# Optimization experiments

Hardware: AMD Instinct MI355X
Metric: run time of the kernel (lower is better)

The kernel has to match this reference:

```python
import jax, jax.numpy as jnp
import numpy as np

H = 64  # hidden_dim

def _gru_cell(x, h, Wih, Whh, bih, bhh):
    # PyTorch GRUCell math: gates ordered (r, z, n)
    gi = x @ Wih.T + bih            # [B, 3H]
    gh = h @ Whh.T + bhh            # [B, 3H]
    i_r, i_z, i_n = jnp.split(gi, 3, axis=-1)
    h_r, h_z, h_n = jnp.split(gh, 3, axis=-1)
    r = jax.nn.sigmoid(i_r + h_r)
    z = jax.nn.sigmoid(i_z + h_z)
    n = jnp.tanh(i_n + r * h_n)
    return (1.0 - z) * n + z * h

def setup_inputs() -> dict:
    key = jax.random.key(0)
    ks = jax.random.split(key, 13)
    B, T, D = 128, 512, 512
    x = jax.random.normal(ks[0], (B, T, D), dtype=jnp.float32)
    s = 1.0 / np.sqrt(H)
    def u(k, shape):
        return jax.random.uniform(k, shape, dtype=jnp.float32, minval=-s, maxval=s)
    return {
        "x": x,
        "W0ih": u(ks[1], (3 * H, D)), "W0hh": u(ks[2], (3 * H, H)),
        "b0ih": u(ks[3], (3 * H,)),   "b0hh": u(ks[4], (3 * H,)),
        "W1ih": u(ks[5], (3 * H, H)), "W1hh": u(ks[6], (3 * H, H)),
        "b1ih": u(ks[7], (3 * H,)),   "b1hh": u(ks[8], (3 * H,)),
        "W2ih": u(ks[9], (3 * H, H)), "W2hh": u(ks[10], (3 * H, H)),
        "b2ih": u(ks[11], (3 * H,)),  "b2hh": u(ks[12], (3 * H,)),
    }

def reference(x, W0ih, W0hh, b0ih, b0hh, W1ih, W1hh, b1ih, b1hh,
              W2ih, W2hh, b2ih, b2hh):
    # bContext=True path: per timestep, if the input slice has any nonzero,
    # run the 3 stacked GRU cells and emit h2; else keep states and emit zeros.
    B = x.shape[0]
    h_init = (jnp.zeros((B, H), x.dtype),) * 3

    def step(carry, xt):  # xt: [B, D]
        h0, h1, h2 = carry
        active = jnp.any(xt != 0)
        n0 = _gru_cell(xt, h0, W0ih, W0hh, b0ih, b0hh)
        n1 = _gru_cell(n0, h1, W1ih, W1hh, b1ih, b1hh)
        n2 = _gru_cell(n1, h2, W2ih, W2hh, b2ih, b2hh)
        h0 = jnp.where(active, n0, h0)
        h1 = jnp.where(active, n1, h1)
        h2 = jnp.where(active, n2, h2)
        out = jnp.where(active, h2, jnp.zeros_like(h2))
        return (h0, h1, h2), out

    xs = jnp.swapaxes(x, 0, 1)          # [T, B, D]
    _, outs = jax.lax.scan(step, h_init, xs)  # [T, B, H]
    return jnp.swapaxes(outs, 0, 1)     # [B, T, H]
```

## Files before the change

kernel.cpp:

```cpp
#include <hip/hip_runtime.h>

#define B_ 128
#define T_ 512
#define D_ 512
#define H_ 64
#define N3 192

#if __has_builtin(__builtin_amdgcn_rcpf)
#define RCP(x) __builtin_amdgcn_rcpf(x)
#else
#define RCP(x) (1.0f / (x))
#endif

typedef _Float16 h2v __attribute__((ext_vector_type(2)));
typedef _Float16 f16x8 __attribute__((ext_vector_type(8)));
typedef float f32x4 __attribute__((ext_vector_type(4)));

__device__ __forceinline__ float sigm_f(float x) {
  return RCP(1.0f + __expf(-x));
}
__device__ __forceinline__ float tanh_f(float x) {
  float e = __expf(-2.0f * fabsf(x));
  float t = (1.0f - e) * RCP(1.0f + e);
  return copysignf(t, x);
}

template <int CTRL>
__device__ __forceinline__ float dpp_add(float v) {
  int t = __builtin_amdgcn_update_dpp(0, __float_as_int(v), CTRL, 0xF, 0xF, true);
  return v + __int_as_float(t);
}
__device__ __forceinline__ float red2(float v) { return dpp_add<0xB1>(v); }
__device__ __forceinline__ float red4(float v) {
  v = dpp_add<0xB1>(v);
  v = dpp_add<0x4E>(v);
  return v;
}

__device__ __forceinline__ void dot4acc(int4 w, int4 h, float& s0, float& s1) {
  s0 = __builtin_amdgcn_fdot2(__builtin_bit_cast(h2v, w.x),
                              __builtin_bit_cast(h2v, h.x), s0, false);
  s1 = __builtin_amdgcn_fdot2(__builtin_bit_cast(h2v, w.y),
                              __builtin_bit_cast(h2v, h.y), s1, false);
  s0 = __builtin_amdgcn_fdot2(__builtin_bit_cast(h2v, w.z),
                              __builtin_bit_cast(h2v, h.z), s0, false);
  s1 = __builtin_amdgcn_fdot2(__builtin_bit_cast(h2v, w.w),
                              __builtin_bit_cast(h2v, h.w), s1, false);
}
__device__ __forceinline__ void dot8reg(const int* w, int4 a, int4 b,
                                        float& s0, float& s1) {
  s0 = __builtin_amdgcn_fdot2(__builtin_bit_cast(h2v, w[0]),
                              __builtin_bit_cast(h2v, a.x), s0, false);
  s1 = __builtin_amdgcn_fdot2(__builtin_bit_cast(h2v, w[1]),
                              __builtin_bit_cast(h2v, a.y), s1, false);
  s0 = __builtin_amdgcn_fdot2(__builtin_bit_cast(h2v, w[2]),
                              __builtin_bit_cast(h2v, a.z), s0, false);
  s1 = __builtin_amdgcn_fdot2(__builtin_bit_cast(h2v, w[3]),
                              __builtin_bit_cast(h2v, a.w), s1, false);
  s0 = __builtin_amdgcn_fdot2(__builtin_bit_cast(h2v, w[4]),
                              __builtin_bit_cast(h2v, b.x), s0, false);
  s1 = __builtin_amdgcn_fdot2(__builtin_bit_cast(h2v, w[5]),
                              __builtin_bit_cast(h2v, b.y), s1, false);
  s0 = __builtin_amdgcn_fdot2(__builtin_bit_cast(h2v, w[6]),
                              __builtin_bit_cast(h2v, b.z), s0, false);
  s1 = __builtin_amdgcn_fdot2(__builtin_bit_cast(h2v, w[7]),
                              __builtin_bit_cast(h2v, b.w), s1, false);
}

#define KEEP(x) asm volatile("" : "+v"(x))

__global__ __launch_bounds__(256) void gemm_kernel(
    const float* __restrict__ x,
    const float* __restrict__ w0ih,
    const float* __restrict__ b0ih,
    float* __restrict__ gi0,
    int* __restrict__ act,
    int t0, int Tc) {
  __shared__ _Float16 Xs[64][72];
  __shared__ _Float16 Ws[64][72];
  __shared__ unsigned char sflag[64];

  const int tid = threadIdx.x;
  const int bid = blockIdx.x;
  const int nt = bid % 3;
  const int mt = bid / 3;
  const int tpc = Tc >> 6;
  const int b  = mt / tpc;
  const int tt = mt % tpc;
  const int c0 = nt * 64;

  const int lane = tid & 63;
  const int wid  = tid >> 6;
  const int wm = (wid >> 1) * 32;
  const int wn = (wid & 1) * 32;
  const int l15 = lane & 15;
  const int l4  = lane >> 4;

  const float* xbase = x + ((size_t)b * T_ + t0 + tt * 64) * D_;
  const float* wbase = w0ih + (size_t)c0 * D_;

  const int srow = tid >> 2;
  const int scg  = (tid & 3) << 4;
  const float* xrow = xbase + (size_t)srow * D_;
  const float* wrow = wbase + (size_t)srow * D_;

  f32x4 acc[2][2];
#pragma unroll
  for (int mi = 0; mi < 2; ++mi)
#pragma unroll
    for (int ni = 0; ni < 2; ++ni) {
      acc[mi][ni].x = 0.f; acc[mi][ni].y = 0.f;
      acc[mi][ni].z = 0.f; acc[mi][ni].w = 0.f;
    }

  bool f = false;

  for (int kt = 0; kt < D_ / 64; ++kt) {
    const int k0 = kt * 64 + scg;
    float4 xa = *(const float4*)&xrow[k0];
    float4 xb = *(const float4*)&xrow[k0 + 4];
    float4 xc = *(const float4*)&xrow[k0 + 8];
    float4 xd = *(const float4*)&xrow[k0 + 12];
    float4 wa = *(const float4*)&wrow[k0];
    float4 wb = *(const float4*)&wrow[k0 + 4];
    float4 wc = *(const float4*)&wrow[k0 + 8];
    float4 wd = *(const float4*)&wrow[k0 + 12];
    f |= (xa.x != 0.f) | (xa.y != 0.f) | (xa.z != 0.f) | (xa.w != 0.f) |
         (xb.x != 0.f) | (xb.y != 0.f) | (xb.z != 0.f) | (xb.w != 0.f) |
         (xc.x != 0.f) | (xc.y != 0.f) | (xc.z != 0.f) | (xc.w != 0.f) |
         (xd.x != 0.f) | (xd.y != 0.f) | (xd.z != 0.f) | (xd.w != 0.f);
    __syncthreads();
    {
      f16x8 p0 = {(_Float16)xa.x, (_Float16)xa.y, (_Float16)xa.z, (_Float16)xa.w,
                  (_Float16)xb.x, (_Float16)xb.y, (_Float16)xb.z, (_Float16)xb.w};
      f16x8 p1 = {(_Float16)xc.x, (_Float16)xc.y, (_Float16)xc.z, (_Float16)xc.w,
                  (_Float16)xd.x, (_Float16)xd.y, (_Float16)xd.z, (_Float16)xd.w};
      *(f16x8*)&Xs[srow][scg] = p0;
      *(f16x8*)&Xs[srow][scg + 8] = p1;
      f16x8 q0 = {(_Float16)wa.x, (_Float16)wa.y, (_Float16)wa.z, (_Float16)wa.w,
                  (_Float16)wb.x, (_Float16)wb.y, (_Float16)wb.z, (_Float16)wb.w};
      f16x8 q1 = {(_Float16)wc.x, (_Float16)wc.y, (_Float16)wc.z, (_Float16)wc.w,
                  (_Float16)wd.x, (_Float16)wd.y, (_Float16)wd.z, (_Float16)wd.w};
      *(f16x8*)&Ws[srow][scg] = q0;
      *(f16x8*)&Ws[srow][scg + 8] = q1;
    }
    __syncthreads();
#pragma unroll
    for (int ks = 0; ks < 2; ++ks) {
      const int kb = ks * 32 + l4 * 8;
      f16x8 a0 = *(const f16x8*)&Xs[wm + l15][kb];
      f16x8 a1 = *(const f16x8*)&Xs[wm + 16 + l15][kb];
      f16x8 b0 = *(const f16x8*)&Ws[wn + l15][kb];
      f16x8 b1 = *(const f16x8*)&Ws[wn + 16 + l15][kb];
      acc[0][0] = __builtin_amdgcn_mfma_f32_16x16x32_f16(a0, b0, acc[0][0], 0, 0, 0);
      acc[0][1] = __builtin_amdgcn_mfma_f32_16x16x32_f16(a0, b1, acc[0][1], 0, 0, 0);
      acc[1][0] = __builtin_amdgcn_mfma_f32_16x16x32_f16(a1, b0, acc[1][0], 0, 0, 0);
      acc[1][1] = __builtin_amdgcn_mfma_f32_16x16x32_f16(a1, b1, acc[1][1], 0, 0, 0);
    }
  }

  const float bias0 = b0ih[c0 + wn + l15];
  const float bias1 = b0ih[c0 + wn + 16 + l15];
  const size_t rowbase = (size_t)b * Tc + tt * 64;
#pragma unroll
  for (int mi = 0; mi < 2; ++mi)
#pragma unroll
    for (int r = 0; r < 4; ++r) {
      const int m = wm + mi * 16 + l4 * 4 + r;
      float* orow = &gi0[(rowbase + m) * N3 + c0 + wn];
      orow[l15]      = acc[mi][0][r] + bias0;
      orow[16 + l15] = acc[mi][1][r] + bias1;
    }

  if (tid < 64) sflag[tid] = 0;
  __syncthreads();
  if (f) sflag[srow] = 1;
  __syncthreads();
  if (tid < 64 && sflag[tid]) act[t0 + tt * 64 + tid] = 1;
}

__global__ __launch_bounds__(640) void scan_kernel(
    const float* __restrict__ gi0,
    const float* __restrict__ w0hh, const float* __restrict__ w1ih,
    const float* __restrict__ w1hh, const float* __restrict__ w2ih,
    const float* __restrict__ w2hh,
    const float* __restrict__ b0hh, const float* __restrict__ b1ih,
    const float* __restrict__ b1hh, const float* __restrict__ b2ih,
    const float* __restrict__ b2hh,
    const int* __restrict__ act,
    float* __restrict__ hstate,
    float* __restrict__ out,
    int t0, int Tc) {
  const int b   = blockIdx.x;
  const int tid = threadIdx.x;

  __shared__ __align__(16) int4 s_w[3][192][8];
  __shared__ __align__(16) _Float16 s_h[3][2][H_];
  __shared__ int s_act[T_];

  {
    const float* wsrc[3] = {w0hh, w1hh, w2hh};
    for (int i = tid; i < 3 * 192 * 8; i += 640) {
      int m = i / 1536;
      int rem = i - m * 1536;
      int row = rem >> 3;
      int c = rem & 7;
      const float* sp = wsrc[m] + (size_t)row * H_ + 8 * c;
      float4 lo = *(const float4*)sp;
      float4 hi = *(const float4*)(sp + 4);
      h2v p0 = {(_Float16)lo.x, (_Float16)lo.y};
      h2v p1 = {(_Float16)lo.z, (_Float16)lo.w};
      h2v p2 = {(_Float16)hi.x, (_Float16)hi.y};
      h2v p3 = {(_Float16)hi.z, (_Float16)hi.w};
      int4 pk;
      pk.x = __builtin_bit_cast(int, p0);
      pk.y = __builtin_bit_cast(int, p1);
      pk.z = __builtin_bit_cast(int, p2);
      pk.w = __builtin_bit_cast(int, p3);
      s_w[m][row][c ^ (row & 7)] = pk;
    }
  }
  for (int i = tid; i < Tc; i += 640) s_act[i] = act[t0 + i];

  const int grp = (tid < 128) ? 0 : (tid < 384) ? 1 : 2;
  const int lt  = tid - ((grp == 0) ? 0 : (grp == 1) ? 128 : 384);
  const int jj  = (grp == 0) ? (lt >> 1) : (lt >> 2);
  const int gg  = (grp == 0) ? (lt & 1) : (lt & 3);
  const int swz = jj & 7;

  if (tid < H_) {
    float v0 = (t0 == 0) ? 0.f : hstate[0 * B_ * H_ + b * H_ + tid];
    float v1 = (t0 == 0) ? 0.f : hstate[1 * B_ * H_ + b * H_ + tid];
    float v2 = (t0 == 0) ? 0.f : hstate[2 * B_ * H_ + b * H_ + tid];
    s_h[0][0][tid] = (_Float16)v0; s_h[0][1][tid] = (_Float16)v0;
    s_h[1][0][tid] = (_Float16)v1; s_h[1][1][tid] = (_Float16)v1;
    s_h[2][0][tid] = (_Float16)v2; s_h[2][1][tid] = (_Float16)v2;
  }
  float hreg = (t0 == 0) ? 0.f : hstate[grp * B_ * H_ + b * H_ + jj];

  int rpk[3][8];
  {
    const float* ihsrc = (grp == 2) ? w2ih : w1ih;
    const int lg = (grp == 0) ? (gg * 2) : gg;
#pragma unroll
    for (int r = 0; r < 3; ++r) {
      const float* src = ihsrc + (size_t)(jj + 64 * r) * H_ + 16 * lg;
#pragma unroll
      for (int q = 0; q < 8; ++q) {
        float2 fv = *(const float2*)(src + 2 * q);
        h2v pv = {(_Float16)fv.x, (_Float16)fv.y};
        rpk[r][q] = __builtin_bit_cast(int, pv);
      }
    }
#pragma unroll
    for (int r = 0; r < 3; ++r)
#pragma unroll
      for (int q = 0; q < 8; ++q) KEEP(rpk[r][q]);
  }

  float bsv[4];
  if (grp == 0) {
    bsv[0] = b0hh[jj]; bsv[1] = b0hh[jj + 64]; bsv[2] = 0.f;
    bsv[3] = b0hh[jj + 128];
  } else if (grp == 1) {
    bsv[0] = b1ih[jj] + b1hh[jj];
    bsv[1] = b1ih[jj + 64] + b1hh[jj + 64];
    bsv[2] = b1ih[jj + 128]; bsv[3] = b1hh[jj + 128];
  } else {
    bsv[0] = b2ih[jj] + b2hh[jj];
    bsv[1] = b2ih[jj + 64] + b2hh[jj + 64];
    bsv[2] = b2ih[jj + 128]; bsv[3] = b2hh[jj + 128];
  }

  const float* gib = gi0 + (size_t)b * Tc * N3;
  float giR = 0.f, giZ = 0.f, giN = 0.f;
  if (grp == 0) { giR = gib[jj]; giZ = gib[jj + 64]; giN = gib[jj + 128]; }

  __syncthreads();

  for (int i = 0; i < Tc + 2; ++i) {
    const int p = i & 1;
    if (grp == 0) {
      if (i < Tc) {
        const int4* hp = (const int4*)s_h[0][p ^ 1];
        int4 h0s = hp[4 * gg + 0], h1s = hp[4 * gg + 1];
        int4 h2s = hp[4 * gg + 2], h3s = hp[4 * gg + 3];
        float R0 = 0, R1 = 0, Z0 = 0, Z1 = 0, N0 = 0, N1 = 0;
#pragma unroll
        for (int k = 0; k < 4; ++k) {
          int pc = (4 * gg + k) ^ swz;
          int4 hk = (k == 0) ? h0s : (k == 1) ? h1s : (k == 2) ? h2s : h3s;
          dot4acc(s_w[0][jj][pc],       hk, R0, R1);
          dot4acc(s_w[0][jj + 64][pc],  hk, Z0, Z1);
          dot4acc(s_w[0][jj + 128][pc], hk, N0, N1);
        }
        float dR = red2(R0 + R1) + bsv[0];
        float dZ = red2(Z0 + Z1) + bsv[1];
        float dN = red2(N0 + N1) + bsv[3];
        bool a = (s_act[i] != 0);
        float r = sigm_f(giR + dR);
        float z = sigm_f(giZ + dZ);
        float n = tanh_f(giN + r * dN);
        float hn = (1.0f - z) * n + z * hreg;
        hreg = a ? hn : hreg;
        if (gg == 0) s_h[0][p][jj] = (_Float16)hreg;
        int tn = (i + 1 < Tc) ? i + 1 : i;
        giR = gib[(size_t)tn * N3 + jj];
        giZ = gib[(size_t)tn * N3 + jj + 64];
        giN = gib[(size_t)tn * N3 + jj + 128];
      }
    } else if (grp == 1) {
      if (i >= 1 && i <= Tc) {
        const int4* h0p = (const int4*)s_h[0][p ^ 1];
        const int4* h1p = (const int4*)s_h[1][p ^ 1];
        int4 x0 = h0p[2 * gg], x1 = h0p[2 * gg + 1];
        int4 y0 = h1p[2 * gg], y1 = h1p[2 * gg + 1];
        float vR0 = 0, vR1 = 0, vZ0 = 0, vZ1 = 0;
        float iN0 = 0, iN1 = 0, hN0 = 0, hN1 = 0;
        dot8reg(rpk[0], x0, x1, vR0, vR1);
        dot8reg(rpk[1], x0, x1, vZ0, vZ1);
        dot8reg(rpk[2], x0, x1, iN0, iN1);
        int pc0 = (2 * gg) ^ swz, pc1 = (2 * gg + 1) ^ swz;
        dot4acc(s_w[1][jj][pc0],       y0, vR0, vR1);
        dot4acc(s_w[1][jj][pc1],       y1, vR0, vR1);
        dot4acc(s_w[1][jj + 64][pc0],  y0, vZ0, vZ1);
        dot4acc(s_w[1][jj + 64][pc1],  y1, vZ0, vZ1);
        dot4acc(s_w[1][jj + 128][pc0], y0, hN0, hN1);
        dot4acc(s_w[1][jj + 128][pc1], y1, hN0, hN1);
        float sR = red4(vR0 + vR1) + bsv[0];
        float sZ = red4(vZ0 + vZ1) + bsv[1];
        float iN = red4(iN0 + iN1) + bsv[2];
        float hN = red4(hN0 + hN1) + bsv[3];
        bool a = (s_act[i - 1] != 0);
        float r = sigm_f(sR);
        float z = sigm_f(sZ);
        float n = tanh_f(iN + r * hN);
        float hn = (1.0f - z) * n + z * hreg;
        hreg = a ? hn : hreg;
        if (gg == 0) s_h[1][p][jj] = (_Float16)hreg;
      }
    } else {
      if (i >= 2) {
        const int4* h1p = (const int4*)s_h[1][p ^ 1];
        const int4* h2p = (const int4*)s_h[2][p ^ 1];
        int4 x0 = h1p[2 * gg], x1 = h1p[2 * gg + 1];
        int4 y0 = h2p[2 * gg], y1 = h2p[2 * gg + 1];
        float vR0 = 0, vR1 = 0, vZ0 = 0, vZ1 = 0;
        float iN0 = 0, iN1 = 0, hN0 = 0, hN1 = 0;
        dot8reg(rpk[0], x0, x1, vR0, vR1);
        dot8reg(rpk[1], x0, x1, vZ0, vZ1);
        dot8reg(rpk[2], x0, x1, iN0, iN1);
        int pc0 = (2 * gg) ^ swz, pc1 = (2 * gg + 1) ^ swz;
        dot4acc(s_w[2][jj][pc0],       y0, vR0, vR1);
        dot4acc(s_w[2][jj][pc1],       y1, vR0, vR1);
        dot4acc(s_w[2][jj + 64][pc0],  y0, vZ0, vZ1);
        dot4acc(s_w[2][jj + 64][pc1],  y1, vZ0, vZ1);
        dot4acc(s_w[2][jj + 128][pc0], y0, hN0, hN1);
        dot4acc(s_w[2][jj + 128][pc1], y1, hN0, hN1);
        float sR = red4(vR0 + vR1) + bsv[0];
        float sZ = red4(vZ0 + vZ1) + bsv[1];
        float iN = red4(iN0 + iN1) + bsv[2];
        float hN = red4(hN0 + hN1) + bsv[3];
        bool a = (s_act[i - 2] != 0);
        float r = sigm_f(sR);
        float z = sigm_f(sZ);
        float n = tanh_f(iN + r * hN);
        float hn = (1.0f - z) * n + z * hreg;
        hreg = a ? hn : hreg;
        if (gg == 0) {
          s_h[2][p][jj] = (_Float16)hreg;
          out[((size_t)b * T_ + t0 + (i - 2)) * H_ + jj] = a ? hreg : 0.0f;
        }
      }
    }
    __syncthreads();
  }

  if (gg == 0) hstate[grp * B_ * H_ + b * H_ + jj] = hreg;
}

extern "C" void kernel_launch(void* const* d_in, const int* in_sizes, int n_in,
                              void* d_out, int out_size, void* d_ws, size_t ws_size,
                              hipStream_t stream) {
  const float* x    = (const float*)d_in[0];
  const float* w0ih = (const float*)d_in[1];
  const float* w0hh = (const float*)d_in[2];
  const float* b0ih = (const float*)d_in[3];
  const float* b0hh = (const float*)d_in[4];
  const float* w1ih = (const float*)d_in[5];
  const float* w1hh = (const float*)d_in[6];
  const float* b1ih = (const float*)d_in[7];
  const float* b1hh = (const float*)d_in[8];
  const float* w2ih = (const float*)d_in[9];
  const float* w2hh = (const float*)d_in[10];
  const float* b2ih = (const float*)d_in[11];
  const float* b2hh = (const float*)d_in[12];
  float* out = (float*)d_out;

  char* p = (char*)d_ws;
  int* act      = (int*)p;    p += 4096;
  float* hstate = (float*)p;  p += (size_t)3 * B_ * H_ * 4;
  size_t fixed = (size_t)(p - (char*)d_ws);

  int Tc = T_;
  while (Tc > 64 && fixed + (size_t)B_ * Tc * N3 * 4 > ws_size) Tc >>= 1;
  float* gi0 = (float*)p;

  hipMemsetAsync(act, 0, T_ * sizeof(int), stream);
  for (int t0 = 0; t0 < T_; t0 += Tc) {
    gemm_kernel<<<dim3(B_ * (Tc / 64) * 3), 256, 0, stream>>>(
        x, w0ih, b0ih, gi0, act, t0, Tc);
    scan_kernel<<<B_, 640, 0, stream>>>(
        gi0, w0hh, w1ih, w1hh, w2ih, w2hh,
        b0hh, b1ih, b1hh, b2ih, b2hh, act, hstate, out, t0, Tc);
  }
}
```

Before: 449.1 us.

## Batch 16 sequences per scan block and compute recurrent gates with MFMA

The scan kernel now processes 16 batch rows per block instead of one, with 12 waves (4 per GRU layer) each computing 16 hidden units via 16x16x32 f16 MFMA, with weights held in registers as B fragments. This replaces per-row fdot2 dot products plus DPP reductions and shared-memory weight reads. The goal is to spread the serial recurrence over tensor cores and cut the per-step instruction count. The trade-off is a grid of only 8 blocks, so most CUs sit idle and latency per step rests on a few CUs.

Result: slower. 596.3 us (+32.8%).

```diff
diff --git a/kernel.cpp b/kernel.cpp
--- a/kernel.cpp
+++ b/kernel.cpp
@@ -5,6 +5,7 @@
 #define D_ 512
 #define H_ 64
 #define N3 192
+#define MB 16
 
 #if __has_builtin(__builtin_amdgcn_rcpf)
 #define RCP(x) __builtin_amdgcn_rcpf(x)
@@ -12,7 +13,6 @@
 #define RCP(x) (1.0f / (x))
 #endif
 
-typedef _Float16 h2v __attribute__((ext_vector_type(2)));
 typedef _Float16 f16x8 __attribute__((ext_vector_type(8)));
 typedef float f32x4 __attribute__((ext_vector_type(4)));
 
@@ -25,49 +25,9 @@
   return copysignf(t, x);
 }
 
-template <int CTRL>
-__device__ __forceinline__ float dpp_add(float v) {
-  int t = __builtin_amdgcn_update_dpp(0, __float_as_int(v), CTRL, 0xF, 0xF, true);
-  return v + __int_as_float(t);
-}
-__device__ __forceinline__ float red2(float v) { return dpp_add<0xB1>(v); }
-__device__ __forceinline__ float red4(float v) {
-  v = dpp_add<0xB1>(v);
-  v = dpp_add<0x4E>(v);
-  return v;
-}
-
-__device__ __forceinline__ void dot4acc(int4 w, int4 h, float& s0, float& s1) {
-  s0 = __builtin_amdgcn_fdot2(__builtin_bit_cast(h2v, w.x),
-                              __builtin_bit_cast(h2v, h.x), s0, false);
-  s1 = __builtin_amdgcn_fdot2(__builtin_bit_cast(h2v, w.y),
-                              __builtin_bit_cast(h2v, h.y), s1, false);
-  s0 = __builtin_amdgcn_fdot2(__builtin_bit_cast(h2v, w.z),
-                              __builtin_bit_cast(h2v, h.z), s0, false);
-  s1 = __builtin_amdgcn_fdot2(__builtin_bit_cast(h2v, w.w),
-                              __builtin_bit_cast(h2v, h.w), s1, false);
-}
-__device__ __forceinline__ void dot8reg(const int* w, int4 a, int4 b,
-                                        float& s0, float& s1) {
-  s0 = __builtin_amdgcn_fdot2(__builtin_bit_cast(h2v, w[0]),
-                              __builtin_bit_cast(h2v, a.x), s0, false);
-  s1 = __builtin_amdgcn_fdot2(__builtin_bit_cast(h2v, w[1]),
-                              __builtin_bit_cast(h2v, a.y), s1, false);
-  s0 = __builtin_amdgcn_fdot2(__builtin_bit_cast(h2v, w[2]),
-                              __builtin_bit_cast(h2v, a.z), s0, false);
-  s1 = __builtin_amdgcn_fdot2(__builtin_bit_cast(h2v, w[3]),
-                              __builtin_bit_cast(h2v, a.w), s1, false);
-  s0 = __builtin_amdgcn_fdot2(__builtin_bit_cast(h2v, w[4]),
-                              __builtin_bit_cast(h2v, b.x), s0, false);
-  s1 = __builtin_amdgcn_fdot2(__builtin_bit_cast(h2v, w[5]),
-                              __builtin_bit_cast(h2v, b.y), s1, false);
-  s0 = __builtin_amdgcn_fdot2(__builtin_bit_cast(h2v, w[6]),
-                              __builtin_bit_cast(h2v, b.z), s0, false);
-  s1 = __builtin_amdgcn_fdot2(__builtin_bit_cast(h2v, w[7]),
-                              __builtin_bit_cast(h2v, b.w), s1, false);
-}
-
 #define KEEP(x) asm volatile("" : "+v"(x))
+#define KEEPV(v) do { int4& kr_ = *reinterpret_cast<int4*>(&(v)); \
+  KEEP(kr_.x); KEEP(kr_.y); KEEP(kr_.z); KEEP(kr_.w); } while (0)
 
 __global__ __launch_bounds__(256) void gemm_kernel(
     const float* __restrict__ x,
@@ -179,7 +139,13 @@
   if (tid < 64 && sflag[tid]) act[t0 + tt * 64 + tid] = 1;
 }
 
-__global__ __launch_bounds__(640) void scan_kernel(
+__device__ __forceinline__ f16x8 loadA(const _Float16* hb, int row, int c) {
+  int pc = c ^ (row & 7);
+  return *(const f16x8*)&hb[row * 64 + 8 * pc];
+}
+#define MFMA16(A, Bv, C) __builtin_amdgcn_mfma_f32_16x16x32_f16(A, Bv, C, 0, 0, 0)
+
+__global__ __launch_bounds__(768, 3) void scan_kernel(
     const float* __restrict__ gi0,
     const float* __restrict__ w0hh, const float* __restrict__ w1ih,
     const float* __restrict__ w1hh, const float* __restrict__ w2ih,
@@ -191,192 +157,184 @@
     float* __restrict__ hstate,
     float* __restrict__ out,
     int t0, int Tc) {
-  const int b   = blockIdx.x;
+  const int b0 = blockIdx.x * MB;
   const int tid = threadIdx.x;
-
-  __shared__ __align__(16) int4 s_w[3][192][8];
-  __shared__ __align__(16) _Float16 s_h[3][2][H_];
+  const int lane = tid & 63;
+  const int wave = tid >> 6;
+  const int grp = wave >> 2;
+  const int w   = wave & 3;
+  const int l15 = lane & 15;
+  const int l4  = lane >> 4;
+  const int j   = 16 * w + l15;
+
+  __shared__ __align__(16) _Float16 s_h[3][2][MB][64];
   __shared__ int s_act[T_];
 
-  {
-    const float* wsrc[3] = {w0hh, w1hh, w2hh};
-    for (int i = tid; i < 3 * 192 * 8; i += 640) {
-      int m = i / 1536;
-      int rem = i - m * 1536;
-      int row = rem >> 3;
-      int c = rem & 7;
-      const float* sp = wsrc[m] + (size_t)row * H_ + 8 * c;
-      float4 lo = *(const float4*)sp;
-      float4 hi = *(const float4*)(sp + 4);
-      h2v p0 = {(_Float16)lo.x, (_Float16)lo.y};
-      h2v p1 = {(_Float16)lo.z, (_Float16)lo.w};
-      h2v p2 = {(_Float16)hi.x, (_Float16)hi.y};
-      h2v p3 = {(_Float16)hi.z, (_Float16)hi.w};
-      int4 pk;
-      pk.x = __builtin_bit_cast(int, p0);
-      pk.y = __builtin_bit_cast(int, p1);
-      pk.z = __builtin_bit_cast(int, p2);
-      pk.w = __builtin_bit_cast(int, p3);
-      s_w[m][row][c ^ (row & 7)] = pk;
-    }
-  }
-  for (int i = tid; i < Tc; i += 640) s_act[i] = act[t0 + i];
-
-  const int grp = (tid < 128) ? 0 : (tid < 384) ? 1 : 2;
-  const int lt  = tid - ((grp == 0) ? 0 : (grp == 1) ? 128 : 384);
-  const int jj  = (grp == 0) ? (lt >> 1) : (lt >> 2);
-  const int gg  = (grp == 0) ? (lt & 1) : (lt & 3);
-  const int swz = jj & 7;
-
-  if (tid < H_) {
-    float v0 = (t0 == 0) ? 0.f : hstate[0 * B_ * H_ + b * H_ + tid];
-    float v1 = (t0 == 0) ? 0.f : hstate[1 * B_ * H_ + b * H_ + tid];
-    float v2 = (t0 == 0) ? 0.f : hstate[2 * B_ * H_ + b * H_ + tid];
-    s_h[0][0][tid] = (_Float16)v0; s_h[0][1][tid] = (_Float16)v0;
-    s_h[1][0][tid] = (_Float16)v1; s_h[1][1][tid] = (_Float16)v1;
-    s_h[2][0][tid] = (_Float16)v2; s_h[2][1][tid] = (_Float16)v2;
-  }
-  float hreg = (t0 == 0) ? 0.f : hstate[grp * B_ * H_ + b * H_ + jj];
-
-  int rpk[3][8];
-  {
-    const float* ihsrc = (grp == 2) ? w2ih : w1ih;
-    const int lg = (grp == 0) ? (gg * 2) : gg;
-#pragma unroll
-    for (int r = 0; r < 3; ++r) {
-      const float* src = ihsrc + (size_t)(jj + 64 * r) * H_ + 16 * lg;
-#pragma unroll
-      for (int q = 0; q < 8; ++q) {
-        float2 fv = *(const float2*)(src + 2 * q);
-        h2v pv = {(_Float16)fv.x, (_Float16)fv.y};
-        rpk[r][q] = __builtin_bit_cast(int, pv);
+  for (int i = tid; i < Tc; i += 768) s_act[i] = act[t0 + i];
+
+  const float* matIH = (grp == 1) ? w1ih : (grp == 2) ? w2ih : w0hh;
+  const float* matHH = (grp == 0) ? w0hh : (grp == 1) ? w1hh : w2hh;
+  f16x8 bf[2][3][2];
+#pragma unroll
+  for (int m2 = 0; m2 < 2; ++m2) {
+    const float* mp = m2 ? matHH : matIH;
+#pragma unroll
+    for (int g = 0; g < 3; ++g)
+#pragma unroll
+      for (int ks = 0; ks < 2; ++ks) {
+        const float* src = mp + (size_t)(64 * g + j) * H_ + l4 * 8 + 32 * ks;
+        f16x8 v;
+#pragma unroll
+        for (int q = 0; q < 8; ++q) v[q] = (_Float16)src[q];
+        bf[m2][g][ks] = v;
       }
-    }
-#pragma unroll
-    for (int r = 0; r < 3; ++r)
-#pragma unroll
-      for (int q = 0; q < 8; ++q) KEEP(rpk[r][q]);
-  }
-
-  float bsv[4];
+  }
+#pragma unroll
+  for (int m2 = 0; m2 < 2; ++m2)
+#pragma unroll
+    for (int g = 0; g < 3; ++g)
+#pragma unroll
+      for (int ks = 0; ks < 2; ++ks) KEEPV(bf[m2][g][ks]);
+
+  float bR, bZ, biN, bhN;
   if (grp == 0) {
-    bsv[0] = b0hh[jj]; bsv[1] = b0hh[jj + 64]; bsv[2] = 0.f;
-    bsv[3] = b0hh[jj + 128];
+    bR = b0hh[j]; bZ = b0hh[j + 64]; biN = 0.f; bhN = b0hh[j + 128];
   } else if (grp == 1) {
-    bsv[0] = b1ih[jj] + b1hh[jj];
-    bsv[1] = b1ih[jj + 64] + b1hh[jj + 64];
-    bsv[2] = b1ih[jj + 128]; bsv[3] = b1hh[jj + 128];
+    bR = b1ih[j] + b1hh[j]; bZ = b1ih[j + 64] + b1hh[j + 64];
+    biN = b1ih[j + 128]; bhN = b1hh[j + 128];
   } else {
-    bsv[0] = b2ih[jj] + b2hh[jj];
-    bsv[1] = b2ih[jj + 64] + b2hh[jj + 64];
-    bsv[2] = b2ih[jj + 128]; bsv[3] = b2hh[jj + 128];
-  }
-
-  const float* gib = gi0 + (size_t)b * Tc * N3;
-  float giR = 0.f, giZ = 0.f, giN = 0.f;
-  if (grp == 0) { giR = gib[jj]; giZ = gib[jj + 64]; giN = gib[jj + 128]; }
+    bR = b2ih[j] + b2hh[j]; bZ = b2ih[j + 64] + b2hh[j + 64];
+    biN = b2ih[j + 128]; bhN = b2hh[j + 128];
+  }
+
+  float hreg[4];
+#pragma unroll
+  for (int r = 0; r < 4; ++r) {
+    int m = l4 * 4 + r;
+    float v = (t0 == 0) ? 0.f
+                        : hstate[grp * B_ * H_ + (size_t)(b0 + m) * H_ + j];
+    hreg[r] = v;
+    int pc = (j >> 3) ^ (m & 7);
+    s_h[grp][0][m][8 * pc + (j & 7)] = (_Float16)v;
+    s_h[grp][1][m][8 * pc + (j & 7)] = (_Float16)v;
+  }
+
+  float giv[3][4];
+  if (grp == 0) {
+#pragma unroll
+    for (int g = 0; g < 3; ++g)
+#pragma unroll
+      for (int r = 0; r < 4; ++r)
+        giv[g][r] = gi0[((size_t)(b0 + l4 * 4 + r) * Tc) * N3 + 64 * g + j];
+  }
 
   __syncthreads();
+
+  const f32x4 zz = {0.f, 0.f, 0.f, 0.f};
 
   for (int i = 0; i < Tc + 2; ++i) {
     const int p = i & 1;
     if (grp == 0) {
       if (i < Tc) {
-        const int4* hp = (const int4*)s_h[0][p ^ 1];
-        int4 h0s = hp[4 * gg + 0], h1s = hp[4 * gg + 1];
-        int4 h2s = hp[4 * gg + 2], h3s = hp[4 * gg + 3];
-        float R0 = 0, R1 = 0, Z0 = 0, Z1 = 0, N0 = 0, N1 = 0;
-#pragma unroll
-        for (int k = 0; k < 4; ++k) {
-          int pc = (4 * gg + k) ^ swz;
-          int4 hk = (k == 0) ? h0s : (k == 1) ? h1s : (k == 2) ? h2s : h3s;
-          dot4acc(s_w[0][jj][pc],       hk, R0, R1);
-          dot4acc(s_w[0][jj + 64][pc],  hk, Z0, Z1);
-          dot4acc(s_w[0][jj + 128][pc], hk, N0, N1);
+        const _Float16* hb = &s_h[0][p ^ 1][0][0];
+        f16x8 a0 = loadA(hb, l15, l4);
+        f16x8 a1 = loadA(hb, l15, l4 + 4);
+        f32x4 aR = MFMA16(a0, bf[1][0][0], zz);
+        aR = MFMA16(a1, bf[1][0][1], aR);
+        f32x4 aZ = MFMA16(a0, bf[1][1][0], zz);
+        aZ = MFMA16(a1, bf[1][1][1], aZ);
+        f32x4 aN = MFMA16(a0, bf[1][2][0], zz);
+        aN = MFMA16(a1, bf[1][2][1], aN);
+        bool a = (s_act[i] != 0);
+#pragma unroll
+        for (int r = 0; r < 4; ++r) {
+          int m = l4 * 4 + r;
+          float R = sigm_f(giv[0][r] + aR[r] + bR);
+          float Z = sigm_f(giv[1][r] + aZ[r] + bZ);
+          float N = tanh_f(giv[2][r] + R * (aN[r] + bhN));
+          float hn = (1.f - Z) * N + Z * hreg[r];
+          hreg[r] = a ? hn : hreg[r];
+          int pc = (j >> 3) ^ (m & 7);
+          s_h[0][p][m][8 * pc + (j & 7)] = (_Float16)hreg[r];
         }
-        float dR = red2(R0 + R1) + bsv[0];
-        float dZ = red2(Z0 + Z1) + bsv[1];
-        float dN = red2(N0 + N1) + bsv[3];
-        bool a = (s_act[i] != 0);
-        float r = sigm_f(giR + dR);
-        float z = sigm_f(giZ + dZ);
-        float n = tanh_f(giN + r * dN);
-        float hn = (1.0f - z) * n + z * hreg;
-        hreg = a ? hn : hreg;
-        if (gg == 0) s_h[0][p][jj] = (_Float16)hreg;
-        int tn = (i + 1 < Tc) ? i + 1 : i;
-        giR = gib[(size_t)tn * N3 + jj];
-        giZ = gib[(size_t)tn * N3 + jj + 64];
-        giN = gib[(size_t)tn * N3 + jj + 128];
+        int tn = (i + 1 < Tc) ? i + 1 : Tc - 1;
+#pragma unroll
+        for (int g = 0; g < 3; ++g)
+#pragma unroll
+          for (int r = 0; r < 4; ++r)
+            giv[g][r] = gi0[((size_t)(b0 + l4 * 4 + r) * Tc + tn) * N3 + 64 * g + j];
       }
     } else if (grp == 1) {
       if (i >= 1 && i <= Tc) {
-        const int4* h0p = (const int4*)s_h[0][p ^ 1];
-        const int4* h1p = (const int4*)s_h[1][p ^ 1];
-        int4 x0 = h0p[2 * gg], x1 = h0p[2 * gg + 1];
-        int4 y0 = h1p[2 * gg], y1 = h1p[2 * gg + 1];
-        float vR0 = 0, vR1 = 0, vZ0 = 0, vZ1 = 0;
-        float iN0 = 0, iN1 = 0, hN0 = 0, hN1 = 0;
-        dot8reg(rpk[0], x0, x1, vR0, vR1);
-        dot8reg(rpk[1], x0, x1, vZ0, vZ1);
-        dot8reg(rpk[2], x0, x1, iN0, iN1);
-        int pc0 = (2 * gg) ^ swz, pc1 = (2 * gg + 1) ^ swz;
-        dot4acc(s_w[1][jj][pc0],       y0, vR0, vR1);
-        dot4acc(s_w[1][jj][pc1],       y1, vR0, vR1);
-        dot4acc(s_w[1][jj + 64][pc0],  y0, vZ0, vZ1);
-        dot4acc(s_w[1][jj + 64][pc1],  y1, vZ0, vZ1);
-        dot4acc(s_w[1][jj + 128][pc0], y0, hN0, hN1);
-        dot4acc(s_w[1][jj + 128][pc1], y1, hN0, hN1);
-        float sR = red4(vR0 + vR1) + bsv[0];
-        float sZ = red4(vZ0 + vZ1) + bsv[1];
-        float iN = red4(iN0 + iN1) + bsv[2];
-        float hN = red4(hN0 + hN1) + bsv[3];
+        const _Float16* hp = &s_h[0][p ^ 1][0][0];
+        const _Float16* hs = &s_h[1][p ^ 1][0][0];
+        f16x8 p0 = loadA(hp, l15, l4), p1 = loadA(hp, l15, l4 + 4);
+        f16x8 s0 = loadA(hs, l15, l4), s1 = loadA(hs, l15, l4 + 4);
+        f32x4 aR = MFMA16(p0, bf[0][0][0], zz);
+        aR = MFMA16(p1, bf[0][0][1], aR);
+        aR = MFMA16(s0, bf[1][0][0], aR);
+        aR = MFMA16(s1, bf[1][0][1], aR);
+        f32x4 aZ = MFMA16(p0, bf[0][1][0], zz);
+        aZ = MFMA16(p1, bf[0][1][1], aZ);
+        aZ = MFMA16(s0, bf[1][1][0], aZ);
+        aZ = MFMA16(s1, bf[1][1][1], aZ);
+        f32x4 aiN = MFMA16(p0, bf[0][2][0], zz);
+        aiN = MFMA16(p1, bf[0][2][1], aiN);
+        f32x4 ahN = MFMA16(s0, bf[1][2][0], zz);
+        ahN = MFMA16(s1, bf[1][2][1], ahN);
         bool a = (s_act[i - 1] != 0);
-        float r = sigm_f(sR);
-        float z = sigm_f(sZ);
-        float n = tanh_f(iN + r * hN);
-        float hn = (1.0f - z) * n + z * hreg;
-        hreg = a ? hn : hreg;
-        if (gg == 0) s_h[1][p][jj] = (_Float16)hreg;
+#pragma unroll
+        for (int r = 0; r < 4; ++r) {
+          int m = l4 * 4 + r;
+          float R = sigm_f(aR[r] + bR);
+          float Z = sigm_f(aZ[r] + bZ);
+          float N = tanh_f(aiN[r] + biN + R * (ahN[r] + bhN));
+          float hn = (1.f - Z) * N + Z * hreg[r];
+          hreg[r] = a ? hn : hreg[r];
+          int pc = (j >> 3) ^ (m & 7);
+          s_h[1][p][m][8 * pc + (j & 7)] = (_Float16)hreg[r];
+        }
       }
     } else {
       if (i >= 2) {
-        const int4* h1p = (const int4*)s_h[1][p ^ 1];
-        const int4* h2p = (const int4*)s_h[2][p ^ 1];
-        int4 x0 = h1p[2 * gg], x1 = h1p[2 * gg + 1];
-        int4 y0 = h2p[2 * gg], y1 = h2p[2 * gg + 1];
-        float vR0 = 0, vR1 = 0, vZ0 = 0, vZ1 = 0;
-        float iN0 = 0, iN1 = 0, hN0 = 0, hN1 = 0;
-        dot8reg(rpk[0], x0, x1, vR0, vR1);
-        dot8reg(rpk[1], x0, x1, vZ0, vZ1);
-        dot8reg(rpk[2], x0, x1, iN0, iN1);
-        int pc0 = (2 * gg) ^ swz, pc1 = (2 * gg + 1) ^ swz;
-        dot4acc(s_w[2][jj][pc0],       y0, vR0, vR1);
-        dot4acc(s_w[2][jj][pc1],       y1, vR0, vR1);
-        dot4acc(s_w[2][jj + 64][pc0],  y0, vZ0, vZ1);
-        dot4acc(s_w[2][jj + 64][pc1],  y1, vZ0, vZ1);
-        dot4acc(s_w[2][jj + 128][pc0], y0, hN0, hN1);
-        dot4acc(s_w[2][jj + 128][pc1], y1, hN0, hN1);
-        float sR = red4(vR0 + vR1) + bsv[0];
-        float sZ = red4(vZ0 + vZ1) + bsv[1];
-        float iN = red4(iN0 + iN1) + bsv[2];
-        float hN = red4(hN0 + hN1) + bsv[3];
+        const _Float16* hp = &s_h[1][p ^ 1][0][0];
+        const _Float16* hs = &s_h[2][p ^ 1][0][0];
+        f16x8 p0 = loadA(hp, l15, l4), p1 = loadA(hp, l15, l4 + 4);
+        f16x8 s0 = loadA(hs, l15, l4), s1 = loadA(hs, l15, l4 + 4);
+        f32x4 aR = MFMA16(p0, bf[0][0][0], zz);
+        aR = MFMA16(p1, bf[0][0][1], aR);
+        aR = MFMA16(s0, bf[1][0][0], aR);
+        aR = MFMA16(s1, bf[1][0][1], aR);
+        f32x4 aZ = MFMA16(p0, bf[0][1][0], zz);
+        aZ = MFMA16(p1, bf[0][1][1], aZ);
+        aZ = MFMA16(s0, bf[1][1][0], aZ);
+        aZ = MFMA16(s1, bf[1][1][1], aZ);
+        f32x4 aiN = MFMA16(p0, bf[0][2][0], zz);
+        aiN = MFMA16(p1, bf[0][2][1], aiN);
+        f32x4 ahN = MFMA16(s0, bf[1][2][0], zz);
+        ahN = MFMA16(s1, bf[1][2][1], ahN);
         bool a = (s_act[i - 2] != 0);
-        float r = sigm_f(sR);
-        float z = sigm_f(sZ);
-        float n = tanh_f(iN + r * hN);
-        float hn = (1.0f - z) * n + z * hreg;
-        hreg = a ? hn : hreg;
-        if (gg == 0) {
-          s_h[2][p][jj] = (_Float16)hreg;
-          out[((size_t)b * T_ + t0 + (i - 2)) * H_ + jj] = a ? hreg : 0.0f;
+        int tcur = t0 + i - 2;
+#pragma unroll
+        for (int r = 0; r < 4; ++r) {
+          int m = l4 * 4 + r;
+          float R = sigm_f(aR[r] + bR);
+          float Z = sigm_f(aZ[r] + bZ);
+          float N = tanh_f(aiN[r] + biN + R * (ahN[r] + bhN));
+          float hn = (1.f - Z) * N + Z * hreg[r];
+          hreg[r] = a ? hn : hreg[r];
+          int pc = (j >> 3) ^ (m & 7);
+          s_h[2][p][m][8 * pc + (j & 7)] = (_Float16)hreg[r];
+          out[((size_t)(b0 + m) * T_ + tcur) * H_ + j] = a ? hreg[r] : 0.f;
         }
       }
     }
     __syncthreads();
   }
 
-  if (gg == 0) hstate[grp * B_ * H_ + b * H_ + jj] = hreg;
+#pragma unroll
+  for (int r = 0; r < 4; ++r)
+    hstate[grp * B_ * H_ + (size_t)(b0 + l4 * 4 + r) * H_ + j] = hreg[r];
 }
 
 extern "C" void kernel_launch(void* const* d_in, const int* in_sizes, int n_in,
@@ -410,7 +368,7 @@
   for (int t0 = 0; t0 < T_; t0 += Tc) {
     gemm_kernel<<<dim3(B_ * (Tc / 64) * 3), 256, 0, stream>>>(
         x, w0ih, b0ih, gi0, act, t0, Tc);
-    scan_kernel<<<B_, 640, 0, stream>>>(
+    scan_kernel<<<B_ / MB, 768, 0, stream>>>(
         gi0, w0hh, w1ih, w1hh, w2ih, w2hh,
         b0hh, b1ih, b1hh, b2ih, b2hh, act, hstate, out, t0, Tc);
   }
```
